# Performance work log

Hardware: AMD Instinct MI355X
Metric: run time of the kernel (lower is better)

Reference implementation:

```python
import jax, jax.numpy as jnp
import numpy as np

ANCHORS = np.array([[10., 13.], [16., 30.], [33., 23.]], dtype=np.float32)
NUM_CLASSES = 80
IMG_W, IMG_H = 416, 416
IGNORE_THR = 0.5
OBJ_SCALE, NOOBJ_SCALE = 1.0, 0.5
EPS = 1e-12


def setup_inputs() -> dict:
    key = jax.random.key(0)
    k1, k2, k3, k4, k5 = jax.random.split(key, 5)
    B, A, C, H, W = 16, 3, NUM_CLASSES, 52, 52
    x = jax.random.normal(k1, (B, A * (C + 5), H, W), dtype=jnp.float32)
    N = 256
    img = jax.random.randint(k2, (N,), 0, B).astype(jnp.float32)
    xy = jax.random.uniform(k3, (N, 2), minval=0.02, maxval=0.98, dtype=jnp.float32)
    wh = jax.random.uniform(k4, (N, 2), minval=0.02, maxval=0.5, dtype=jnp.float32)
    cls = jax.random.randint(k5, (N,), 0, C).astype(jnp.float32)
    target = jnp.concatenate([img[:, None], xy, wh, cls[:, None]], axis=1)
    return {"x": x, "target": target}


def _masked_mse(p, t, m):
    n = jnp.maximum(jnp.sum(m), 1.0)
    return jnp.sum(m * (p - t) ** 2) / n


def _masked_bce(p, t, m):
    p = jnp.clip(p, EPS, 1.0 - EPS)
    n = jnp.maximum(jnp.sum(m), 1.0)
    return jnp.sum(m * (-(t * jnp.log(p) + (1.0 - t) * jnp.log(1.0 - p)))) / n


def _yolo(x, target):
    anchors = jnp.asarray(ANCHORS)
    B, A, C = x.shape[0], anchors.shape[0], NUM_CLASSES
    H, W = x.shape[2], x.shape[3]
    stride_h, stride_w = IMG_H / H, IMG_W / W
    # [B, A, H, W, C+5]
    pred = x.reshape(B, A, C + 5, H, W).transpose(0, 1, 3, 4, 2)
    cx = jax.nn.sigmoid(pred[..., 0])
    cy = jax.nn.sigmoid(pred[..., 1])
    pw = pred[..., 2]
    ph = pred[..., 3]
    pconf = jax.nn.sigmoid(pred[..., 4])
    pcls = jax.nn.sigmoid(pred[..., 5:])

    # ---- detect (boxes use .data in torch -> stop_gradient) ----
    grid_x = jnp.arange(W, dtype=jnp.float32)[None, None, None, :]
    grid_y = jnp.arange(H, dtype=jnp.float32)[None, None, :, None]
    scale_aw = (anchors[:, 0] / stride_w).reshape(1, A, 1, 1)
    scale_ah = (anchors[:, 1] / stride_h).reshape(1, A, 1, 1)
    bx = jax.lax.stop_gradient(cx) + grid_x
    by = jax.lax.stop_gradient(cy) + grid_y
    bw = jnp.exp(jax.lax.stop_gradient(pw)) * scale_aw
    bh = jnp.exp(jax.lax.stop_gradient(ph)) * scale_ah
    boxes = jnp.stack([bx * stride_w, by * stride_h, bw * stride_w, bh * stride_h], -1)
    output = jnp.concatenate(
        [boxes.reshape(B, -1, 4), pconf.reshape(B, -1, 1), pcls.reshape(B, -1, C)], -1)

    # ---- build targets ----
    img_num = target[:, 0].astype(jnp.int32)
    gxc = target[:, 1] * W
    gyc = target[:, 2] * H
    gw = target[:, 3] * W
    gh = target[:, 4] * H
    label = target[:, 5].astype(jnp.int32)
    # wh-IoU of raw pixel anchors vs grid-unit gt (faithful to original, which
    # passes unscaled self.anchors to bbox_wh_iou)
    aw = anchors[:, 0][:, None]  # [A,1]
    ah = anchors[:, 1][:, None]
    inter = jnp.minimum(aw, gw[None, :]) * jnp.minimum(ah, gh[None, :])
    ious = inter / (aw * ah + 1e-16 + gw[None, :] * gh[None, :] - inter)  # [A,N]
    best_index = jnp.argmax(ious, axis=0)  # [N]
    gi = gxc.astype(jnp.int32)
    gj = gyc.astype(jnp.int32)

    shp = (B, A, H, W)
    obj_mask = jnp.zeros(shp, jnp.float32).at[img_num, best_index, gj, gi].set(1.0)
    noobj_mask = jnp.ones(shp, jnp.float32).at[img_num, best_index, gj, gi].set(0.0)
    # zero noobj where any anchor IoU > ignore threshold
    N = target.shape[0]
    anc = jnp.broadcast_to(jnp.arange(A, dtype=jnp.int32)[:, None], (A, N))
    img_b = jnp.broadcast_to(img_num[None, :], (A, N))
    gj_b = jnp.broadcast_to(gj[None, :], (A, N))
    gi_b = jnp.broadcast_to(gi[None, :], (A, N))
    keep = jnp.where(ious > IGNORE_THR, 0.0, 1.0)
    noobj_mask = noobj_mask.at[img_b, anc, gj_b, gi_b].min(keep)

    tx = jnp.zeros(shp, jnp.float32).at[img_num, best_index, gj, gi].set(gxc - jnp.floor(gxc))
    ty = jnp.zeros(shp, jnp.float32).at[img_num, best_index, gj, gi].set(gyc - jnp.floor(gyc))
    tw = jnp.zeros(shp, jnp.float32).at[img_num, best_index, gj, gi].set(
        jnp.log(gw / anchors[best_index, 0] + 1e-16))
    th = jnp.zeros(shp, jnp.float32).at[img_num, best_index, gj, gi].set(
        jnp.log(gh / anchors[best_index, 1] + 1e-16))
    tconf = jnp.zeros(shp, jnp.float32).at[img_num, best_index, gj, gi].set(1.0)
    tcls = jnp.zeros(shp + (C,), jnp.float32).at[img_num, best_index, gj, gi, label].set(1.0)

    # ---- masked losses (replicating original's center_x/self.w bugs) ----
    loss_x = _masked_mse(cx, tx, obj_mask)
    loss_y = _masked_mse(cx, ty, obj_mask)   # original uses center_x for y loss
    loss_w = _masked_mse(pw, tw, obj_mask)
    loss_h = _masked_mse(pw, th, obj_mask)   # original uses self.w for h loss
    loss_conf = (OBJ_SCALE * _masked_bce(pconf, tconf, obj_mask)
                 + NOOBJ_SCALE * _masked_bce(pconf, tconf, noobj_mask))
    cls_mask = jnp.broadcast_to(obj_mask[..., None], tcls.shape)
    loss_cls = _masked_bce(pcls, tcls, cls_mask)
    total = loss_x + loss_y + loss_w + loss_h + loss_conf + loss_cls
    return output, total


def reference(x, target):
    return _yolo(x, target)
```

## Files before the change

kernel.cpp:

```cpp
#include <hip/hip_runtime.h>
#include <math.h>

#define NA 3
#define NC 80
#define CH 85
#define NB 16
#define HH 52
#define WW 52
#define HW 2704
#define HWF4 676
#define NT 256
#define NCELLS (NB*NA*HW)
#define NBMW 4056
#define STRIDE_F 8.0f
#define IGN_THR 0.5f

#define TP 104
#define TF4 26
#define NF4 2210
#define LSTR 105
#define LDSW 8945
#define NDENSE 1248

#define NWINB 64
#define NZEROB 3
#define TAILB (NWINB + NZEROB)
#define GRID_B (TAILB + NDENSE)

#define SW(c, l) ((c) * LSTR + (l) + ((c) >> 2))

__device__ __forceinline__ float sigm(float z) { return 1.0f / (1.0f + expf(-z)); }
__device__ __forceinline__ float splus(float z) { return log1pf(expf(z)); }


__global__ __launch_bounds__(256) void prep_kernel(
        const float* __restrict__ target, float* __restrict__ acc,
        int* __restrict__ cnts, int* __restrict__ wofs,
        float* __restrict__ wtx, float* __restrict__ wty,
        float* __restrict__ wtw, float* __restrict__ wth,
        int* __restrict__ wlabel, int* __restrict__ zofs) {
    __shared__ int plds[NBMW + NT + 2];
    unsigned int* bm = (unsigned int*)plds;
    int* s_keyobj = plds + NBMW;
    int* s_cnt = plds + NBMW + NT;
    int t = threadIdx.x;

    if (t < 16) acc[t] = 0.0f;
    if (t == 0) { s_cnt[0] = 0; s_cnt[1] = 0; }
    for (int i = t; i < NBMW; i += 256) bm[i] = 0u;

    const float awc[3] = {10.f, 16.f, 33.f};
    const float ahc[3] = {13.f, 30.f, 23.f};
    float timg = target[t*6 + 0];
    float gxc  = target[t*6 + 1] * (float)WW;
    float gyc  = target[t*6 + 2] * (float)HH;
    float gw   = target[t*6 + 3] * (float)WW;
    float gh   = target[t*6 + 4] * (float)HH;
    int label  = (int)target[t*6 + 5];

    float best_iou = -1.0f;
    int best = 0, ignbits = 0;
    for (int a = 0; a < 3; a++) {
        float inter = fminf(awc[a], gw) * fminf(ahc[a], gh);
        float iou = inter / (awc[a]*ahc[a] + 1e-16f + gw*gh - inter);
        if (iou > best_iou) { best_iou = iou; best = a; }
        if (iou > IGN_THR) ignbits |= (1 << a);
    }
    int img = (int)timg;
    int gi = (int)gxc, gj = (int)gyc;
    int pixel = gj * WW + gi;
    int cellbase = img * (NA * HW) + pixel;
    int keyobj = cellbase + best * HW;
    s_keyobj[t] = keyobj;
    __syncthreads();

    bool dup = false;
    #pragma unroll 8
    for (int m = 0; m < NT; m++) {
        int k = s_keyobj[m];
        dup = dup || (m > t && k == keyobj);
    }
    if (!dup) {
        int p = atomicAdd(&s_cnt[0], 1);
        wofs[p] = (img * NA + best) * (CH * HW) + pixel;
        wtx[p] = gxc - floorf(gxc);
        wty[p] = gyc - floorf(gyc);
        wtw[p] = logf(gw / awc[best] + 1e-16f);
        wth[p] = logf(gh / ahc[best] + 1e-16f);
        wlabel[p] = label;
    }
    for (int a = 0; a < 3; a++) {
        bool flag = (a == best) || ((ignbits >> a) & 1);
        if (flag) {
            int key = cellbase + a * HW;
            unsigned int bit = 1u << (key & 31);
            unsigned int old = atomicOr(&bm[key >> 5], bit);
            if (!(old & bit)) {
                int p = atomicAdd(&s_cnt[1], 1);
                zofs[p] = ((img * NA + a) * CH + 4) * HW + pixel;
            }
        }
    }
    __syncthreads();
    if (t == 0) { cnts[0] = s_cnt[0]; cnts[1] = s_cnt[1]; }
}

__global__ __launch_bounds__(256) void main_kernel(
        const float* __restrict__ x, float* __restrict__ out,
        float* __restrict__ acc, const int* __restrict__ cnts,
        const int* __restrict__ wofs, const float* __restrict__ wtx,
        const float* __restrict__ wty, const float* __restrict__ wtw,
        const float* __restrict__ wth, const int* __restrict__ wlabel,
        const int* __restrict__ zofs, float* __restrict__ partials) {
    __shared__ float lds[LDSW];
    __shared__ float red[4];
    int bid = blockIdx.x;
    int t = threadIdx.x;

    if (bid >= TAILB) {
        int dbid  = bid - TAILB;
        int chunk = dbid % 26;
        int ba    = dbid / 26;
        int a     = ba % NA;
        const float awc[3] = {10.f, 16.f, 33.f};
        const float ahc[3] = {13.f, 30.f, 23.f};

        const float4* x4 = (const float4*)x + (size_t)ba * (CH * HWF4)
                                            + chunk * TF4;
        float4 v[9];
        #pragma unroll
        for (int i = 0; i < 9; i++) {
            int idx = t + i * 256;
            if (idx < NF4) {
                int c = idx / TF4, q = idx - c * TF4;
                v[i] = x4[c * HWF4 + q];
            }
        }
        float noobj = 0.0f;
        #pragma unroll
        for (int i = 0; i < 9; i++) {
            int idx = t + i * 256;
            if (idx < NF4) {
                int c = idx / TF4, q = idx - c * TF4;
                float r[4] = {v[i].x, v[i].y, v[i].z, v[i].w};
                #pragma unroll
                for (int k = 0; k < 4; k++) {
                    int l = q * 4 + k;
                    float z = r[k], o;
                    if (c == 0) {
                        int wc = l - ((l >= WW) ? WW : 0);
                        o = (sigm(z) + (float)wc) * STRIDE_F;
                    } else if (c == 1) {
                        int hc = chunk * 2 + ((l >= WW) ? 1 : 0);
                        o = (sigm(z) + (float)hc) * STRIDE_F;
                    } else if (c == 2) {
                        o = expf(z) * awc[a];
                    } else if (c == 3) {
                        o = expf(z) * ahc[a];
                    } else {
                        o = sigm(z);
                        if (c == 4) noobj += splus(z);
                    }
                    lds[SW(c, l)] = o;
                }
            }
        }
        for (int off = 32; off > 0; off >>= 1)
            noobj += __shfl_down(noobj, off, 64);
        if ((t & 63) == 0) red[t >> 6] = noobj;
        __syncthreads();

        float4* o4 = (float4*)out + (size_t)ba * (HW * CH / 4) + chunk * NF4;
        #pragma unroll
        for (int i = 0; i < 9; i++) {
            int j = t + i * 256;
            if (j < NF4) {
                int flat = 4 * j;
                int cell = flat / CH;
                int ch = flat - cell * CH;
                float4 w;
                float* pw = &w.x;
                #pragma unroll
                for (int k = 0; k < 4; k++) {
                    int chk = ch + k, cek = cell;
                    if (chk >= CH) { chk -= CH; cek += 1; }
                    pw[k] = lds[SW(chk, cek)];
                }
                o4[j] = w;
            }
        }
        if (t == 0) partials[dbid] = red[0] + red[1] + red[2] + red[3];
        return;
    }

    if (bid < NWINB) {
        int wave = t >> 6, lane = t & 63;
        int w = bid * 4 + wave;
        if (w < cnts[0]) {
            int ofs = wofs[w];
            int label = wlabel[w];
            const float* xp = x + ofs;
            float lcls;
            {
                float z = xp[(size_t)(5 + lane) * HW];
                lcls = (lane == label) ? splus(-z) : splus(z);
            }
            if (lane < 16) {
                int c = 64 + lane;
                float z = xp[(size_t)(5 + c) * HW];
                lcls += (c == label) ? splus(-z) : splus(z);
            }
            float other = 0.0f;
            if (lane == 0) {
                float z0 = xp[0];
                float z2 = xp[(size_t)2 * HW];
                float z4 = xp[(size_t)4 * HW];
                float cx = sigm(z0);
                float dx = cx - wtx[w], dy = cx - wty[w];
                float dw = z2 - wtw[w], dh = z2 - wth[w];
                other = dx*dx + dy*dy + dw*dw + dh*dh + splus(-z4);
            }
            for (int off = 32; off > 0; off >>= 1)
                lcls += __shfl_down(lcls, off, 64);
            if (lane == 0) {
                atomicAdd(&acc[1], other);
                atomicAdd(&acc[2], lcls);
            }
        }
    } else {
        int idx = (bid - NWINB) * 256 + t;
        float vv = 0.0f;
        if (idx < cnts[1]) vv = splus(x[zofs[idx]]);
        for (int off = 32; off > 0; off >>= 1)
            vv += __shfl_down(vv, off, 64);
        if ((t & 63) == 0) atomicAdd(&acc[3], vv);
    }
}

__global__ __launch_bounds__(256) void finalize_kernel(
        const float* __restrict__ partials, const float* __restrict__ acc,
        const int* __restrict__ cnts, float* __restrict__ out_total) {
    __shared__ float red[4];
    int t = threadIdx.x;
    float s = 0.0f;
    for (int i = t; i < NDENSE; i += 256) s += partials[i];
    for (int off = 32; off > 0; off >>= 1)
        s += __shfl_down(s, off, 64);
    if ((t & 63) == 0) red[t >> 6] = s;
    __syncthreads();
    if (t == 0) {
        float a0 = red[0] + red[1] + red[2] + red[3];
        float a1 = acc[1], a2 = acc[2], a3 = acc[3];
        float wc = (float)cnts[0];
        float zc = (float)cnts[1];
        float n_obj = fmaxf(wc, 1.0f);
        float n_noobj = fmaxf((float)NCELLS - zc, 1.0f);
        float cls_den = fmaxf(80.0f * wc, 1.0f);
        out_total[0] = a1 / n_obj + a2 / cls_den
                     + 0.5f * ((a0 - a3) / n_noobj);
    }
}

extern "C" void kernel_launch(void* const* d_in, const int* in_sizes, int n_in,
                              void* d_out, int out_size, void* d_ws, size_t ws_size,
                              hipStream_t stream) {
    (void)in_sizes; (void)n_in; (void)out_size; (void)ws_size;
    const float* x      = (const float*)d_in[0];
    const float* target = (const float*)d_in[1];
    float* out = (float*)d_out;

    char* ws = (char*)d_ws;
    float* acc      = (float*)(ws + 0);
    int*   cnts     = (int*)  (ws + 64);
    int*   wofs     = (int*)  (ws + 128);
    float* wtx      = (float*)(ws + 1152);
    float* wty      = (float*)(ws + 2176);
    float* wtw      = (float*)(ws + 3200);
    float* wth      = (float*)(ws + 4224);
    int*   wlabel   = (int*)  (ws + 5248);
    int*   zofs     = (int*)  (ws + 6272);
    float* partials = (float*)(ws + 9344);

    prep_kernel<<<1, 256, 0, stream>>>(
        target, acc, cnts, wofs, wtx, wty, wtw, wth, wlabel, zofs);
    main_kernel<<<GRID_B, 256, 0, stream>>>(
        x, out, acc, cnts, wofs, wtx, wty, wtw, wth, wlabel, zofs, partials);
    finalize_kernel<<<1, 256, 0, stream>>>(
        partials, acc, cnts, out + (size_t)NB * NA * HW * CH);
}
```

Before: 124.2 us.

## Split dense transpose into per-wave 16-pixel tiles with XOR-swizzled LDS

The dense output transpose moves from block-wide 104-pixel chunks to independent per-wave tiles of 16 pixels. Each wave loads 85 channels by 16 pixels, writes them to its own LDS region with an XOR swizzle, and writes out the interleaved result after only a wave barrier. This removes the block-wide __syncthreads, keeps less data in registers and LDS per block, and creates more blocks for latency hiding. The cost is shorter contiguous runs on global reads (64 bytes per channel row), more partial sums for the finalize kernel to reduce, and per-element div/mod to compute grid coordinates.

```diff
diff --git a/kernel.cpp b/kernel.cpp
--- a/kernel.cpp
+++ b/kernel.cpp
@@ -15,19 +15,19 @@
 #define STRIDE_F 8.0f
 #define IGN_THR 0.5f
 
-#define TP 104
-#define TF4 26
-#define NF4 2210
-#define LSTR 105
-#define LDSW 8945
-#define NDENSE 1248
+#define NTILE_BA 169
+#define NWTILES (NTILE_BA*NB*NA)
+#define NDBLK (NWTILES/4)
+#define S2 88
+#define WLDS (16*S2)
+#define NF4C 340
 
 #define NWINB 64
 #define NZEROB 3
 #define TAILB (NWINB + NZEROB)
-#define GRID_B (TAILB + NDENSE)
-
-#define SW(c, l) ((c) * LSTR + (l) + ((c) >> 2))
+#define GRID_B (TAILB + NDBLK)
+
+__device__ __forceinline__ int swz(int a) { return a ^ (((a >> 5) & 7) << 2); }
 
 __device__ __forceinline__ float sigm(float z) { return 1.0f / (1.0f + expf(-z)); }
 __device__ __forceinline__ float splus(float z) { return log1pf(expf(z)); }
@@ -112,47 +112,46 @@
         const float* __restrict__ wty, const float* __restrict__ wtw,
         const float* __restrict__ wth, const int* __restrict__ wlabel,
         const int* __restrict__ zofs, float* __restrict__ partials) {
-    __shared__ float lds[LDSW];
-    __shared__ float red[4];
+    __shared__ float lds[4 * WLDS];
     int bid = blockIdx.x;
     int t = threadIdx.x;
 
     if (bid >= TAILB) {
-        int dbid  = bid - TAILB;
-        int chunk = dbid % 26;
-        int ba    = dbid / 26;
-        int a     = ba % NA;
+        int lane = t & 63;
+        int wt = (bid - TAILB) * 4 + (t >> 6);
+        int ba = wt / NTILE_BA;
+        int tile = wt - ba * NTILE_BA;
+        int a = ba % NA;
         const float awc[3] = {10.f, 16.f, 33.f};
         const float ahc[3] = {13.f, 30.f, 23.f};
+        float* wl = &lds[(t >> 6) * WLDS];
 
         const float4* x4 = (const float4*)x + (size_t)ba * (CH * HWF4)
-                                            + chunk * TF4;
-        float4 v[9];
+                                            + tile * 4;
+        float4 v[6];
         #pragma unroll
-        for (int i = 0; i < 9; i++) {
-            int idx = t + i * 256;
-            if (idx < NF4) {
-                int c = idx / TF4, q = idx - c * TF4;
-                v[i] = x4[c * HWF4 + q];
-            }
+        for (int i = 0; i < 6; i++) {
+            int c = i * 16 + (lane >> 2);
+            if (c < CH) v[i] = x4[(size_t)c * HWF4 + (lane & 3)];
         }
         float noobj = 0.0f;
         #pragma unroll
-        for (int i = 0; i < 9; i++) {
-            int idx = t + i * 256;
-            if (idx < NF4) {
-                int c = idx / TF4, q = idx - c * TF4;
+        for (int i = 0; i < 6; i++) {
+            int c = i * 16 + (lane >> 2);
+            if (c < CH) {
                 float r[4] = {v[i].x, v[i].y, v[i].z, v[i].w};
                 #pragma unroll
                 for (int k = 0; k < 4; k++) {
-                    int l = q * 4 + k;
+                    int cell = 4 * (lane & 3) + k;
                     float z = r[k], o;
                     if (c == 0) {
-                        int wc = l - ((l >= WW) ? WW : 0);
-                        o = (sigm(z) + (float)wc) * STRIDE_F;
+                        int gpix = tile * 16 + cell;
+                        int px = gpix % WW;
+                        o = (sigm(z) + (float)px) * STRIDE_F;
                     } else if (c == 1) {
-                        int hc = chunk * 2 + ((l >= WW) ? 1 : 0);
-                        o = (sigm(z) + (float)hc) * STRIDE_F;
+                        int gpix = tile * 16 + cell;
+                        int py = gpix / WW;
+                        o = (sigm(z) + (float)py) * STRIDE_F;
                     } else if (c == 2) {
                         o = expf(z) * awc[a];
                     } else if (c == 3) {
@@ -161,35 +160,35 @@
                         o = sigm(z);
                         if (c == 4) noobj += splus(z);
                     }
-                    lds[SW(c, l)] = o;
+                    wl[swz(cell * S2 + c)] = o;
                 }
             }
         }
-        for (int off = 32; off > 0; off >>= 1)
-            noobj += __shfl_down(noobj, off, 64);
-        if ((t & 63) == 0) red[t >> 6] = noobj;
-        __syncthreads();
-
-        float4* o4 = (float4*)out + (size_t)ba * (HW * CH / 4) + chunk * NF4;
+        __builtin_amdgcn_wave_barrier();
+
+        float4* o4 = (float4*)out + (size_t)ba * (HW * CH / 4)
+                                  + tile * NF4C;
         #pragma unroll
-        for (int i = 0; i < 9; i++) {
-            int j = t + i * 256;
-            if (j < NF4) {
+        for (int i = 0; i < 6; i++) {
+            int j = lane + i * 64;
+            if (j < NF4C) {
                 int flat = 4 * j;
-                int cell = flat / CH;
-                int ch = flat - cell * CH;
+                int ce = flat / CH;
+                int c0 = flat - ce * CH;
                 float4 w;
                 float* pw = &w.x;
                 #pragma unroll
                 for (int k = 0; k < 4; k++) {
-                    int chk = ch + k, cek = cell;
-                    if (chk >= CH) { chk -= CH; cek += 1; }
-                    pw[k] = lds[SW(chk, cek)];
+                    int ch = c0 + k, cek = ce;
+                    if (ch >= CH) { ch -= CH; cek += 1; }
+                    pw[k] = wl[swz(cek * S2 + ch)];
                 }
                 o4[j] = w;
             }
         }
-        if (t == 0) partials[dbid] = red[0] + red[1] + red[2] + red[3];
+        for (int off = 32; off > 0; off >>= 1)
+            noobj += __shfl_down(noobj, off, 64);
+        if (lane == 0) partials[wt] = noobj;
         return;
     }
 
@@ -243,7 +242,7 @@
     __shared__ float red[4];
     int t = threadIdx.x;
     float s = 0.0f;
-    for (int i = t; i < NDENSE; i += 256) s += partials[i];
+    for (int i = t; i < NWTILES; i += 256) s += partials[i];
     for (int off = 32; off > 0; off >>= 1)
         s += __shfl_down(s, off, 64);
     if ((t & 63) == 0) red[t >> 6] = s;
```

Result: slower. 137.6 us (+10.8%).

## Fuse finalize into main kernel via last-block atomic counter and cap dense grid

Applied to the files above, without the earlier changes.

Removes the separate finalize kernel launch: each block atomically adds its noobj partial and increments a done counter, and the last block computes the total loss. The dense-tile grid is capped at 1024 slots, with blocks looping over the remaining tiles, so the grid fits better on the CUs. This saves one launch and the partials buffer round trip. In exchange it adds global atomics per block and a serial second pass for some blocks, and the result depends on atomic ordering for memory visibility.

```diff
diff --git a/kernel.cpp b/kernel.cpp
--- a/kernel.cpp
+++ b/kernel.cpp
@@ -21,11 +21,12 @@
 #define LSTR 105
 #define LDSW 8945
 #define NDENSE 1248
+#define NDSLOT 1024
 
 #define NWINB 64
 #define NZEROB 3
 #define TAILB (NWINB + NZEROB)
-#define GRID_B (TAILB + NDENSE)
+#define GRID_B (TAILB + NDSLOT)
 
 #define SW(c, l) ((c) * LSTR + (l) + ((c) >> 2))
 
@@ -46,6 +47,7 @@
     int t = threadIdx.x;
 
     if (t < 16) acc[t] = 0.0f;
+    if (t == 16) cnts[3] = 0;
     if (t == 0) { s_cnt[0] = 0; s_cnt[1] = 0; }
     for (int i = t; i < NBMW; i += 256) bm[i] = 0u;
 
@@ -107,89 +109,111 @@
 
 __global__ __launch_bounds__(256) void main_kernel(
         const float* __restrict__ x, float* __restrict__ out,
-        float* __restrict__ acc, const int* __restrict__ cnts,
+        float* acc, const int* __restrict__ cnts, int* done,
         const int* __restrict__ wofs, const float* __restrict__ wtx,
         const float* __restrict__ wty, const float* __restrict__ wtw,
         const float* __restrict__ wth, const int* __restrict__ wlabel,
-        const int* __restrict__ zofs, float* __restrict__ partials) {
+        const int* __restrict__ zofs, float* __restrict__ out_total) {
     __shared__ float lds[LDSW];
     __shared__ float red[4];
     int bid = blockIdx.x;
     int t = threadIdx.x;
 
     if (bid >= TAILB) {
-        int dbid  = bid - TAILB;
-        int chunk = dbid % 26;
-        int ba    = dbid / 26;
-        int a     = ba % NA;
         const float awc[3] = {10.f, 16.f, 33.f};
         const float ahc[3] = {13.f, 30.f, 23.f};
-
-        const float4* x4 = (const float4*)x + (size_t)ba * (CH * HWF4)
-                                            + chunk * TF4;
-        float4 v[9];
-        #pragma unroll
-        for (int i = 0; i < 9; i++) {
-            int idx = t + i * 256;
-            if (idx < NF4) {
-                int c = idx / TF4, q = idx - c * TF4;
-                v[i] = x4[c * HWF4 + q];
-            }
-        }
-        float noobj = 0.0f;
-        #pragma unroll
-        for (int i = 0; i < 9; i++) {
-            int idx = t + i * 256;
-            if (idx < NF4) {
-                int c = idx / TF4, q = idx - c * TF4;
-                float r[4] = {v[i].x, v[i].y, v[i].z, v[i].w};
-                #pragma unroll
-                for (int k = 0; k < 4; k++) {
-                    int l = q * 4 + k;
-                    float z = r[k], o;
-                    if (c == 0) {
-                        int wc = l - ((l >= WW) ? WW : 0);
-                        o = (sigm(z) + (float)wc) * STRIDE_F;
-                    } else if (c == 1) {
-                        int hc = chunk * 2 + ((l >= WW) ? 1 : 0);
-                        o = (sigm(z) + (float)hc) * STRIDE_F;
-                    } else if (c == 2) {
-                        o = expf(z) * awc[a];
-                    } else if (c == 3) {
-                        o = expf(z) * ahc[a];
-                    } else {
-                        o = sigm(z);
-                        if (c == 4) noobj += splus(z);
+        float blk_noobj = 0.0f;
+        for (int dtile = bid - TAILB; dtile < NDENSE; dtile += NDSLOT) {
+            if (dtile != bid - TAILB) __syncthreads();
+            int chunk = dtile % 26;
+            int ba    = dtile / 26;
+            int a     = ba % NA;
+
+            const float4* x4 = (const float4*)x + (size_t)ba * (CH * HWF4)
+                                                + chunk * TF4;
+            float4 v[9];
+            #pragma unroll
+            for (int i = 0; i < 9; i++) {
+                int idx = t + i * 256;
+                if (idx < NF4) {
+                    int c = idx / TF4, q = idx - c * TF4;
+                    v[i] = x4[c * HWF4 + q];
+                }
+            }
+            float noobj = 0.0f;
+            #pragma unroll
+            for (int i = 0; i < 9; i++) {
+                int idx = t + i * 256;
+                if (idx < NF4) {
+                    int c = idx / TF4, q = idx - c * TF4;
+                    float r[4] = {v[i].x, v[i].y, v[i].z, v[i].w};
+                    #pragma unroll
+                    for (int k = 0; k < 4; k++) {
+                        int l = q * 4 + k;
+                        float z = r[k], o;
+                        if (c == 0) {
+                            int wc = l - ((l >= WW) ? WW : 0);
+                            o = (sigm(z) + (float)wc) * STRIDE_F;
+                        } else if (c == 1) {
+                            int hc = chunk * 2 + ((l >= WW) ? 1 : 0);
+                            o = (sigm(z) + (float)hc) * STRIDE_F;
+                        } else if (c == 2) {
+                            o = expf(z) * awc[a];
+                        } else if (c == 3) {
+                            o = expf(z) * ahc[a];
+                        } else {
+                            o = sigm(z);
+                            if (c == 4) noobj += splus(z);
+                        }
+                        lds[SW(c, l)] = o;
                     }
-                    lds[SW(c, l)] = o;
                 }
             }
-        }
-        for (int off = 32; off > 0; off >>= 1)
-            noobj += __shfl_down(noobj, off, 64);
-        if ((t & 63) == 0) red[t >> 6] = noobj;
-        __syncthreads();
-
-        float4* o4 = (float4*)out + (size_t)ba * (HW * CH / 4) + chunk * NF4;
-        #pragma unroll
-        for (int i = 0; i < 9; i++) {
-            int j = t + i * 256;
-            if (j < NF4) {
-                int flat = 4 * j;
-                int cell = flat / CH;
-                int ch = flat - cell * CH;
-                float4 w;
-                float* pw = &w.x;
-                #pragma unroll
-                for (int k = 0; k < 4; k++) {
-                    int chk = ch + k, cek = cell;
-                    if (chk >= CH) { chk -= CH; cek += 1; }
-                    pw[k] = lds[SW(chk, cek)];
+            for (int off = 32; off > 0; off >>= 1)
+                noobj += __shfl_down(noobj, off, 64);
+            if ((t & 63) == 0) red[t >> 6] = noobj;
+            __syncthreads();
+
+            float4* o4 = (float4*)out + (size_t)ba * (HW * CH / 4)
+                                      + chunk * NF4;
+            #pragma unroll
+            for (int i = 0; i < 9; i++) {
+                int j = t + i * 256;
+                if (j < NF4) {
+                    int flat = 4 * j;
+                    int cell = flat / CH;
+                    int ch = flat - cell * CH;
+                    float4 w;
+                    float* pw = &w.x;
+                    #pragma unroll
+                    for (int k = 0; k < 4; k++) {
+                        int chk = ch + k, cek = cell;
+                        if (chk >= CH) { chk -= CH; cek += 1; }
+                        pw[k] = lds[SW(chk, cek)];
+                    }
+                    o4[j] = w;
                 }
-                o4[j] = w;
-            }
-        }
-        if (t == 0) partials[dbid] = red[0] + red[1] + red[2] + red[3];
+            }
+            if (t == 0) blk_noobj += red[0] + red[1] + red[2] + red[3];
+        }
+        if (t == 0) {
+            float old = atomicAdd(&acc[0], blk_noobj);
+            asm volatile("" :: "v"(old) : "memory");
+            int o = atomicAdd(done, 1);
+            if (o == GRID_B - 1) {
+                float a0 = atomicAdd(&acc[0], 0.0f);
+                float a1 = atomicAdd(&acc[1], 0.0f);
+                float a2 = atomicAdd(&acc[2], 0.0f);
+                float a3 = atomicAdd(&acc[3], 0.0f);
+                float wc = (float)cnts[0];
+                float zc = (float)cnts[1];
+                float n_obj = fmaxf(wc, 1.0f);
+                float n_noobj = fmaxf((float)NCELLS - zc, 1.0f);
+                float cls_den = fmaxf(80.0f * wc, 1.0f);
+                out_total[0] = a1 / n_obj + a2 / cls_den
+                             + 0.5f * ((a0 - a3) / n_noobj);
+            }
+        }
         return;
     }
 
@@ -223,8 +247,9 @@
             for (int off = 32; off > 0; off >>= 1)
                 lcls += __shfl_down(lcls, off, 64);
             if (lane == 0) {
-                atomicAdd(&acc[1], other);
-                atomicAdd(&acc[2], lcls);
+                float o1 = atomicAdd(&acc[1], other);
+                float o2 = atomicAdd(&acc[2], lcls);
+                asm volatile("" :: "v"(o1), "v"(o2) : "memory");
             }
         }
     } else {
@@ -233,31 +258,28 @@
         if (idx < cnts[1]) vv = splus(x[zofs[idx]]);
         for (int off = 32; off > 0; off >>= 1)
             vv += __shfl_down(vv, off, 64);
-        if ((t & 63) == 0) atomicAdd(&acc[3], vv);
-    }
-}
-
-__global__ __launch_bounds__(256) void finalize_kernel(
-        const float* __restrict__ partials, const float* __restrict__ acc,
-        const int* __restrict__ cnts, float* __restrict__ out_total) {
-    __shared__ float red[4];
-    int t = threadIdx.x;
-    float s = 0.0f;
-    for (int i = t; i < NDENSE; i += 256) s += partials[i];
-    for (int off = 32; off > 0; off >>= 1)
-        s += __shfl_down(s, off, 64);
-    if ((t & 63) == 0) red[t >> 6] = s;
+        if ((t & 63) == 0) {
+            float o3 = atomicAdd(&acc[3], vv);
+            asm volatile("" :: "v"(o3) : "memory");
+        }
+    }
+
     __syncthreads();
     if (t == 0) {
-        float a0 = red[0] + red[1] + red[2] + red[3];
-        float a1 = acc[1], a2 = acc[2], a3 = acc[3];
-        float wc = (float)cnts[0];
-        float zc = (float)cnts[1];
-        float n_obj = fmaxf(wc, 1.0f);
-        float n_noobj = fmaxf((float)NCELLS - zc, 1.0f);
-        float cls_den = fmaxf(80.0f * wc, 1.0f);
-        out_total[0] = a1 / n_obj + a2 / cls_den
-                     + 0.5f * ((a0 - a3) / n_noobj);
+        int o = atomicAdd(done, 1);
+        if (o == GRID_B - 1) {
+            float a0 = atomicAdd(&acc[0], 0.0f);
+            float a1 = atomicAdd(&acc[1], 0.0f);
+            float a2 = atomicAdd(&acc[2], 0.0f);
+            float a3 = atomicAdd(&acc[3], 0.0f);
+            float wc = (float)cnts[0];
+            float zc = (float)cnts[1];
+            float n_obj = fmaxf(wc, 1.0f);
+            float n_noobj = fmaxf((float)NCELLS - zc, 1.0f);
+            float cls_den = fmaxf(80.0f * wc, 1.0f);
+            out_total[0] = a1 / n_obj + a2 / cls_den
+                         + 0.5f * ((a0 - a3) / n_noobj);
+        }
     }
 }
 
@@ -279,12 +301,10 @@
     float* wth      = (float*)(ws + 4224);
     int*   wlabel   = (int*)  (ws + 5248);
     int*   zofs     = (int*)  (ws + 6272);
-    float* partials = (float*)(ws + 9344);
 
     prep_kernel<<<1, 256, 0, stream>>>(
         target, acc, cnts, wofs, wtx, wty, wtw, wth, wlabel, zofs);
     main_kernel<<<GRID_B, 256, 0, stream>>>(
-        x, out, acc, cnts, wofs, wtx, wty, wtw, wth, wlabel, zofs, partials);
-    finalize_kernel<<<1, 256, 0, stream>>>(
-        partials, acc, cnts, out + (size_t)NB * NA * HW * CH);
+        x, out, acc, cnts, &cnts[3], wofs, wtx, wty, wtw, wth, wlabel, zofs,
+        out + (size_t)NB * NA * HW * CH);
 }
```

Measured after the change: 130.2 us. 1.05x slower.
